# Performance work log

Measured on AMD Instinct MI355X. Metric: run time of the kernel, lower is better.

Reference implementation:

```python
import jax, jax.numpy as jnp
import numpy as np

V = 25; NE = 5; DIM = 192; H = 6; HD = 32; N = 64; T = 64
SCALE = HD ** -0.5
COEFF = 0.4
NTU_EDGES = [(1,2),(2,21),(3,21),(4,3),(5,21),(6,5),(7,6),(8,7),(9,21),(10,9),(11,10),(12,11),(13,1),(14,13),(15,14),(16,15),(17,1),(18,17),(19,18),(20,19),(22,23),(23,8),(24,25),(25,12)]

def _compute_hops():
    # replicate MHSA.__init__ hop-distance computation (A = [I, adj, adj] summed+binarized)
    adj = np.zeros((V, V))
    for i, j in NTU_EDGES:
        adj[i-1, j-1] = 1.0; adj[j-1, i-1] = 1.0
    h1 = ((np.eye(V) + adj) != 0).astype(np.float64)
    h = [None] * V
    h[0] = np.eye(V); h[1] = h1
    hops = np.zeros((V, V))
    for i in range(2, V):
        h[i] = ((h[i-1] @ h1.T) != 0).astype(np.float64)
    for i in range(V-1, 0, -1):
        if np.any(h[i] - h[i-1]):
            h[i] = h[i] - h[i-1]
            hops += i * h[i]
    return hops.astype(np.int32)

def setup_inputs() -> dict:
    key = jax.random.key(0)
    ks = jax.random.split(key, 12)
    hops = jnp.asarray(_compute_hops())
    n_hop = int(hops.max()) + 1
    std = 0.02
    return {
        "x": jax.random.normal(ks[0], (N, DIM, T, V), jnp.float32),
        "joint_label": jnp.arange(V, dtype=jnp.int32) % NE,  # all 5 hyperedge labels present
        "groups": NE,  # unused by forward (kept for signature fidelity)
        "he_weight": jax.random.uniform(ks[1], (NE,), jnp.float32),
        "hops": hops,
        "ln_g": jnp.ones((DIM,), jnp.float32),
        "ln_b": jnp.zeros((DIM,), jnp.float32),
        "hgc_w": std * jax.random.normal(ks[2], (DIM, DIM), jnp.float32),
        "q_w": std * jax.random.normal(ks[3], (DIM, DIM), jnp.float32),
        "kv_w": std * jax.random.normal(ks[4], (2 * DIM, DIM), jnp.float32),
        "proj_w": std * jax.random.normal(ks[5], (DIM, HD), jnp.float32),  # grouped 1x1 conv, groups=6
        "proj_b": jnp.zeros((DIM,), jnp.float32),
        "rpe": std * jax.random.normal(ks[6], (n_hop, DIM), jnp.float32),
        "w1": std * jax.random.normal(ks[7], (H, HD), jnp.float32),
        "outer": jnp.tile(jnp.eye(V, dtype=jnp.float32), (H, 1, 1)) + std * jax.random.normal(ks[8], (H, V, V), jnp.float32),
        "alpha": 0.1 * jnp.ones((1,), jnp.float32),
        "lin1_w": std * jax.random.normal(ks[9], (T // 5, T), jnp.float32),
        "lin1_b": jnp.zeros((T // 5,), jnp.float32),
        "lin2_w": std * jax.random.normal(ks[10], (T, T // 5), jnp.float32),
        "lin2_b": jnp.zeros((T,), jnp.float32),
    }

def _forward(x, joint_label, he_weight, hops, ln_g, ln_b, hgc_w, q_w, kv_w, proj_w, proj_b, rpe, w1, outer, alpha, lin1_w, lin1_b, lin2_w, lin2_b):
    N_, C, T_, V_ = x.shape
    # ---- HGattn branch: hypergraph conv + temporal squeeze-excite gate ----
    label = jax.nn.one_hot(joint_label, NE, dtype=x.dtype)            # (V, 5)
    label1 = label / label.sum(0, keepdims=True)
    label1 = label1 / jnp.sqrt(label.sum(1, keepdims=True))
    label1 = (he_weight[None, :] * label1).T                          # (5, V)
    norm_label = label / label.sum(1, keepdims=True)
    h_adj = norm_label @ label1                                       # (V, V)
    z = jnp.einsum('nctv,vw->nctw', x, h_adj)
    op = jnp.einsum('nctv,oc->notv', z, hgc_w)                        # (N, dim, T, V) 1x1 conv
    op_tr = op.transpose(0, 1, 3, 2)                                  # (N, dim, V, T)
    s = op_tr.mean(axis=(1, 2))                                       # (N, T) global avg pool over (dim, V)
    g = jax.nn.sigmoid(jax.nn.relu(s @ lin1_w.T + lin1_b) @ lin2_w.T + lin2_b)  # (N, T)
    op_final = op_tr + COEFF * (op_tr * g[:, None, None, :])
    e = op_final.transpose(0, 1, 3, 2)                                # (N, dim, T, V)
    # ---- LayerNorm over channel dim ----
    xc = x.transpose(0, 2, 3, 1)                                      # (N, T, V, C)
    mu = xc.mean(-1, keepdims=True)
    var = xc.var(-1, keepdims=True)
    xn = (((xc - mu) / jnp.sqrt(var + 1e-5)) * ln_g + ln_b).transpose(0, 3, 1, 2)
    # ---- MHSA with hop-indexed relative bias, e-branch scores, outer fusion ----
    q = jnp.einsum('nctv,oc->notv', xn, q_w).reshape(N_, H, HD, T_, V_).transpose(0, 3, 1, 4, 2)   # (N,T,H,V,hd)
    kv = jnp.einsum('nctv,oc->notv', xn, kv_w).reshape(N_, 2, H, HD, T_, V_)
    k = kv[:, 0].transpose(0, 3, 1, 4, 2)
    v = kv[:, 1].transpose(0, 3, 1, 4, 2)
    e_k = e.reshape(N_, H, HD, T_, V_).transpose(0, 3, 1, 4, 2)
    k_r = rpe[hops].reshape(V_, V_, H, HD)                            # hop-distance relative position table
    b = jnp.einsum('bthnc,nmhc->bthnm', q, k_r)
    c = jnp.einsum('bthnc,bthmc->bthnm', q, e_k)
    d = jnp.einsum('hc,bthmc->bthm', w1, e_k)[..., None, :]
    a = jnp.einsum('bthnc,bthmc->bthnm', q, k)
    attn = jax.nn.softmax((a + b + c + d) * SCALE, axis=-1)
    o = jnp.einsum('bthnm,bthmc->bthnc', alpha * attn + outer[None, None], v)
    o = o.transpose(0, 1, 2, 4, 3).reshape(N_, T_, DIM, V_).transpose(0, 2, 1, 3)  # (N, dim, T, V)
    # grouped 1x1 conv projection (groups = H)
    og = o.reshape(N_, H, HD, T_, V_)
    wg = proj_w.reshape(H, HD, HD)
    o = jnp.einsum('ngitv,goi->ngotv', og, wg).reshape(N_, DIM, T_, V_) + proj_b[None, :, None, None]
    return x + o  # dim_in == dim -> identity skip

def reference(x, joint_label, groups, he_weight, hops, ln_g, ln_b, hgc_w, q_w, kv_w, proj_w, proj_b, rpe, w1, outer, alpha, lin1_w, lin1_b, lin2_w, lin2_b):
    return _forward(x, joint_label, he_weight, hops, ln_g, ln_b, hgc_w, q_w, kv_w, proj_w, proj_b, rpe, w1, outer, alpha, lin1_w, lin1_b, lin2_w, lin2_b)
```

## Files before the change

### kernel.cpp

```cpp
#include <hip/hip_runtime.h>
#include <hip/hip_bf16.h>

using bf16 = __hip_bfloat16;
typedef __bf16 bf16x8 __attribute__((ext_vector_type(8)));
typedef float f32x4 __attribute__((ext_vector_type(4)));

constexpr int kDim = 192;
constexpr int kH = 6;
constexpr int kHd = 32;
constexpr int kN = 64;
constexpr int kT = 64;
constexpr int kV = 25;
constexpr int kP = kT * kV;
constexpr int kNCstride = kDim * kP;
constexpr float kScale = 0.17677669529663687f;
constexpr float kCoeff = 0.4f;

__global__ void __launch_bounds__(256) setup_kernel(
    const int* __restrict__ jl, const float* __restrict__ hew,
    const float* __restrict__ hgc, const float* __restrict__ qw,
    const float* __restrict__ kvw, const float* __restrict__ rpe,
    const float* __restrict__ proj_w, const float* __restrict__ lng,
    const float* __restrict__ lnb, int n_hop, float* __restrict__ hadj,
    bf16* __restrict__ Wb, float* __restrict__ G, float* __restrict__ Bb,
    bf16* __restrict__ RPEb, bf16* __restrict__ pwb, bf16* __restrict__ VT) {
  const int bid = blockIdx.x;
  const int tid = threadIdx.x;
  if (bid < 576) {
    int i = bid * 256 + tid;
    float v;
    if (i < 36864) {
      v = hgc[i];
    } else {
      int local = i - 36864;
      int c = local % kDim;
      v = (local < 36864) ? qw[local] : kvw[local - 36864];
      v *= lng[c];
    }
    Wb[i] = __float2bfloat16(v);
  } else if (bid == 576) {
    __shared__ int lbl[kV];
    __shared__ int cnt[8];
    if (tid < 8) cnt[tid] = 0;
    __syncthreads();
    if (tid < kV) { lbl[tid] = jl[tid]; atomicAdd(&cnt[lbl[tid]], 1); }
    __syncthreads();
    for (int idx = tid; idx < kV * kV; idx += 256) {
      int v = idx / kV, w = idx - v * kV;
      float val = 0.f;
      if (lbl[v] == lbl[w]) val = hew[lbl[v]] / (float)cnt[lbl[v]];
      hadj[idx] = val;
    }
  } else if (bid == 577) {
    for (int i = tid; i < kH * 16 * kHd; i += 256) {
      int h = i >> 9, hp = (i >> 5) & 15, d = i & 31;
      float v = (hp < n_hop) ? rpe[hp * kDim + h * kHd + d] : 0.f;
      RPEb[i] = __float2bfloat16(v);
    }
    for (int i = tid; i < kDim * kHd; i += 256)
      pwb[i] = __float2bfloat16(proj_w[i]);
  } else if (bid < 722) {
    int o = (bid - 578) * 4 + (tid >> 6);
    int lane = tid & 63;
    const float* Wr =
        (o < kDim) ? (qw + (size_t)o * kDim) : (kvw + (size_t)(o - kDim) * kDim);
    float gs = 0.f, bs = 0.f;
    for (int c = lane; c < kDim; c += 64) {
      float wv = Wr[c];
      gs += wv * lng[c];
      bs += wv * lnb[c];
    }
    for (int off = 32; off > 0; off >>= 1) {
      gs += __shfl_down(gs, off);
      bs += __shfl_down(bs, off);
    }
    if (lane == 0) { G[o] = gs; Bb[o] = bs; }
  } else {
    int row = (bid - 722) * 256 + tid;
    if (row < kN * kT * kDim) {
      uint4 z = {0u, 0u, 0u, 0u};
      *reinterpret_cast<uint4*>(reinterpret_cast<char*>(VT) + (size_t)row * 64 +
                                48) = z;
    }
  }
}

__global__ void __launch_bounds__(256) prep_kernel(
    const float* __restrict__ x, bf16* __restrict__ XR, float* __restrict__ mu,
    float* __restrict__ rstd) {
  __shared__ float ps[kV][25], ps2[kV][25];
  const int tid = threadIdx.x;
  const int t = blockIdx.x, n = blockIdx.y;
  const float* xb = x + (size_t)n * kNCstride + t * kV;
  size_t ob = ((size_t)n * kP + t * kV) * kDim;
  for (int idx = tid; idx < 600; idx += 256) {
    int p = idx % 25, c8 = idx / 25;
    float a = 0.f, b = 0.f;
    union { uint4 u; __bf16 h[8]; } pk;
#pragma unroll
    for (int i = 0; i < 8; ++i) {
      float v = xb[(size_t)(c8 * 8 + i) * kP + p];
      a += v;
      b += v * v;
      pk.h[i] = (__bf16)v;
    }
    *reinterpret_cast<uint4*>(XR + ob + (size_t)p * kDim + c8 * 8) = pk.u;
    ps[p][c8] = a;
    ps2[p][c8] = b;
  }
  __syncthreads();
  if (tid < kV) {
    float a = 0.f, b = 0.f;
#pragma unroll
    for (int c8 = 0; c8 < 24; ++c8) { a += ps[tid][c8]; b += ps2[tid][c8]; }
    float m = a * (1.f / kDim);
    float var = b * (1.f / kDim) - m * m;
    int gid = n * kP + t * kV + tid;
    mu[gid] = m;
    rstd[gid] = rsqrtf(var + 1e-5f);
  }
}

__global__ void __launch_bounds__(64) gemm_all_kernel(
    const bf16* __restrict__ A, const bf16* __restrict__ B,
    bf16* __restrict__ OP, bf16* __restrict__ QK, bf16* __restrict__ VT,
    const float* __restrict__ muA, const float* __restrict__ rsA,
    const float* __restrict__ G, const float* __restrict__ Bb) {
  int id = blockIdx.x;
  int per = gridDim.x >> 3;
  int wg = (id & 7) * per + (id >> 3);
  int n = wg / 300;
  int rem = wg - n * 300;
  const int pt = rem / 12;
  const int ob = rem % 12;
  const int pb = pt * 64;
  const int l = threadIdx.x;
  B += (size_t)n * kNCstride;
  f32x4 acc[4][4] = {};
  const int lm = l & 15;
  const int lk = (l >> 4) * 8;
  for (int kb = 0; kb < kDim; kb += 32) {
    bf16x8 af[4], bfv[4];
#pragma unroll
    for (int mf = 0; mf < 4; ++mf)
      af[mf] = *reinterpret_cast<const bf16x8*>(
          A + (size_t)(ob * 64 + mf * 16 + lm) * kDim + kb + lk);
#pragma unroll
    for (int nf = 0; nf < 4; ++nf)
      bfv[nf] = *reinterpret_cast<const bf16x8*>(
          B + (size_t)(pb + nf * 16 + lm) * kDim + kb + lk);
#pragma unroll
    for (int mf = 0; mf < 4; ++mf)
#pragma unroll
      for (int nf = 0; nf < 4; ++nf)
        acc[mf][nf] = __builtin_amdgcn_mfma_f32_16x16x32_bf16(
            af[mf], bfv[nf], acc[mf][nf], 0, 0, 0);
  }
  const int r0 = (l >> 4) * 4;
  if (ob < 3) {
    OP += (size_t)n * kP * kDim;
#pragma unroll
    for (int mf = 0; mf < 4; ++mf) {
      const int o0 = ob * 64 + mf * 16 + r0;
#pragma unroll
      for (int nf = 0; nf < 4; ++nf) {
        const int p = pb + nf * 16 + lm;
        union { uint2 u; bf16 b[4]; } pk;
#pragma unroll
        for (int r = 0; r < 4; ++r) pk.b[r] = __float2bfloat16(acc[mf][nf][r]);
        *reinterpret_cast<uint2*>(OP + (size_t)p * kDim + o0) = pk.u;
      }
    }
    return;
  }
  float rsv[4], muv[4];
  int tt[4], vv[4];
#pragma unroll
  for (int nf = 0; nf < 4; ++nf) {
    int p = pb + nf * 16 + lm;
    rsv[nf] = rsA[n * kP + p];
    muv[nf] = muA[n * kP + p];
    tt[nf] = p / 25;
    vv[nf] = p - tt[nf] * 25;
  }
#pragma unroll
  for (int mf = 0; mf < 4; ++mf) {
    const int oq = ob * 64 - 192 + mf * 16 + r0;
    float4 g4 = *reinterpret_cast<const float4*>(G + oq);
    float4 b4 = *reinterpret_cast<const float4*>(Bb + oq);
    float ga[4] = {g4.x, g4.y, g4.z, g4.w};
    float ba[4] = {b4.x, b4.y, b4.z, b4.w};
    if (ob < 9) {
#pragma unroll
      for (int nf = 0; nf < 4; ++nf) {
        const int p = pb + nf * 16 + lm;
        union { uint2 u; bf16 b[4]; } pk;
#pragma unroll
        for (int r = 0; r < 4; ++r)
          pk.b[r] = __float2bfloat16(
              rsv[nf] * (acc[mf][nf][r] - muv[nf] * ga[r]) + ba[r]);
        *reinterpret_cast<uint2*>(QK + ((size_t)n * kP + p) * 384 + oq) = pk.u;
      }
    } else {
#pragma unroll
      for (int nf = 0; nf < 4; ++nf) {
        size_t rowb =
            ((size_t)(n * kT + tt[nf]) * kDim + (oq - 384)) * 32 + vv[nf];
#pragma unroll
        for (int r = 0; r < 4; ++r) {
          float vvv = rsv[nf] * (acc[mf][nf][r] - muv[nf] * ga[r]) + ba[r];
          VT[rowb + (size_t)r * 32] = __float2bfloat16(vvv);
        }
      }
    }
  }
}

__global__ void __launch_bounds__(256) haapply_kernel(
    bf16* __restrict__ OP, const float* __restrict__ hadjg,
    float* __restrict__ s_out) {
  __shared__ ushort tile[kV * kDim];
  __shared__ float ha[640];
  __shared__ float red[4];
  const int tid = threadIdx.x;
  const int t = blockIdx.x, n = blockIdx.y;
  size_t base = ((size_t)n * kP + t * kV) * kDim;
  for (int i = tid; i < kV * kV; i += 256) ha[i] = hadjg[i];
  const uint2* src = reinterpret_cast<const uint2*>(OP + base);
  uint2* dst2 = reinterpret_cast<uint2*>(tile);
  for (int i = tid; i < kV * kDim / 4; i += 256) dst2[i] = src[i];
  __syncthreads();
  float ssum = 0.f;
  for (int idx = tid; idx < 600; idx += 256) {
    int c8 = idx % 24, w = idx / 24;
    float acc[8] = {0.f, 0.f, 0.f, 0.f, 0.f, 0.f, 0.f, 0.f};
    for (int v = 0; v < kV; ++v) {
      float coef = ha[v * kV + w];
      union { uint4 u; __bf16 h[8]; } ld;
      ld.u = *reinterpret_cast<const uint4*>(tile + v * kDim + c8 * 8);
#pragma unroll
      for (int j = 0; j < 8; ++j) acc[j] += coef * (float)ld.h[j];
    }
    union { uint4 u; __bf16 h[8]; } pk;
    float s8 = 0.f;
#pragma unroll
    for (int j = 0; j < 8; ++j) { pk.h[j] = (__bf16)acc[j]; s8 += acc[j]; }
    *reinterpret_cast<uint4*>(OP + base + (size_t)w * kDim + c8 * 8) = pk.u;
    ssum += s8;
  }
  for (int off = 32; off > 0; off >>= 1) ssum += __shfl_down(ssum, off);
  if ((tid & 63) == 0) red[tid >> 6] = ssum;
  __syncthreads();
  if (tid == 0)
    s_out[n * kT + t] = (red[0] + red[1] + red[2] + red[3]) *
                        (1.f / (float)(kDim * kV));
}

__global__ void gate_kernel(const float* __restrict__ s,
                            const float* __restrict__ w1l,
                            const float* __restrict__ b1,
                            const float* __restrict__ w2l,
                            const float* __restrict__ b2,
                            float* __restrict__ gatef) {
  __shared__ float sh[kT];
  __shared__ float hid[12];
  int n = blockIdx.x, t = threadIdx.x;
  sh[t] = s[n * kT + t];
  __syncthreads();
  if (t < 12) {
    float a = b1[t];
    for (int j = 0; j < kT; ++j) a += sh[j] * w1l[t * kT + j];
    hid[t] = fmaxf(a, 0.f);
  }
  __syncthreads();
  float a = b2[t];
  for (int j = 0; j < 12; ++j) a += hid[j] * w2l[t * 12 + j];
  float g = 1.f / (1.f + __expf(-a));
  gatef[n * kT + t] = 1.f + kCoeff * g;
}

__global__ void __launch_bounds__(384) attn_kernel(
    const bf16* __restrict__ QK, const bf16* __restrict__ VT,
    const bf16* __restrict__ OP, const float* __restrict__ gatef,
    const int* __restrict__ hops, const bf16* __restrict__ RPEb,
    const float* __restrict__ w1, const float* __restrict__ outer,
    const float* __restrict__ alpha_p, const bf16* __restrict__ pwb,
    const float* __restrict__ proj_b, const float* __restrict__ x,
    float* __restrict__ out) {
  __shared__ ushort wls[kH][2304];
  const int tid = threadIdx.x;
  const int lane = tid & 63;
  const int h = tid >> 6;
  const int t = blockIdx.x, n = blockIdx.y;
  const int nt = n * kT + t;
  const int lm = lane & 15, g = lane >> 4;
  const bool w1ok = (lm + 16) < kV;

  bf16* Pp = (bf16*)&wls[h][0];
  bf16* OLp = (bf16*)&wls[h][1152];

  const float f = gatef[nt];
  const float alpha = alpha_p[0];
  const bf16* Qbase = QK + (size_t)(nt * kV) * 384;
  const bf16* Ebase = OP + (size_t)(nt * kV) * kDim;
  const int colO = h * kHd + g * 8;

  bf16x8 qf[2], kf[2], ef[2];
#pragma unroll
  for (int mf = 0; mf < 2; ++mf) {
    const bf16* row = Qbase + (size_t)(mf * 16 + lm) * 384;
    qf[mf] = *reinterpret_cast<const bf16x8*>(row + colO);
    kf[mf] = *reinterpret_cast<const bf16x8*>(row + kDim + colO);
    ef[mf] = *reinterpret_cast<const bf16x8*>(
        Ebase + (size_t)(mf * 16 + lm) * kDim + colO);
  }
  bf16x8 rf = *reinterpret_cast<const bf16x8*>(RPEb + (h * 16 + lm) * kHd + g * 8);
  bf16x8 vb[2], pwf[2];
#pragma unroll
  for (int nf = 0; nf < 2; ++nf) {
    vb[nf] = *reinterpret_cast<const bf16x8*>(
        VT + ((size_t)(nt * kDim + h * kHd + nf * 16 + lm)) * 32 + g * 8);
    pwf[nf] = *reinterpret_cast<const bf16x8*>(
        pwb + (h * kHd + nf * 16 + lm) * kHd + g * 8);
  }

  float w1v[8];
  {
    float4 wa = *reinterpret_cast<const float4*>(w1 + h * kHd + g * 8);
    float4 wb = *reinterpret_cast<const float4*>(w1 + h * kHd + g * 8 + 4);
    w1v[0] = wa.x; w1v[1] = wa.y; w1v[2] = wa.z; w1v[3] = wa.w;
    w1v[4] = wb.x; w1v[5] = wb.y; w1v[6] = wb.z; w1v[7] = wb.w;
  }
  float dt[2];
#pragma unroll
  for (int nf = 0; nf < 2; ++nf) {
    float a = 0.f;
#pragma unroll
    for (int j = 0; j < 8; ++j) a += w1v[j] * (float)ef[nf][j];
    a += __shfl_xor(a, 16);
    a += __shfl_xor(a, 32);
    dt[nf] = f * a;
  }

  bf16x8 kef[2];
#pragma unroll
  for (int nf = 0; nf < 2; ++nf)
#pragma unroll
    for (int j = 0; j < 8; ++j)
      kef[nf][j] = (__bf16)((float)kf[nf][j] + f * (float)ef[nf][j]);

  f32x4 aK[2][2] = {};
  f32x4 aR[2] = {};
#pragma unroll
  for (int mf = 0; mf < 2; ++mf) {
#pragma unroll
    for (int nf = 0; nf < 2; ++nf)
      aK[mf][nf] =
          __builtin_amdgcn_mfma_f32_16x16x32_bf16(qf[mf], kef[nf], aK[mf][nf], 0, 0, 0);
    aR[mf] = __builtin_amdgcn_mfma_f32_16x16x32_bf16(qf[mf], rf, aR[mf], 0, 0, 0);
  }

#pragma unroll
  for (int mf = 0; mf < 2; ++mf) {
#pragma unroll
    for (int r = 0; r < 4; ++r) {
      int v = mf * 16 + g * 4 + r;
      int vc = v < kV ? v : kV - 1;
      int hp0 = hops[vc * kV + lm];
      int hp1 = w1ok ? hops[vc * kV + lm + 16] : 0;
      float qr0 = __shfl(aR[mf][r], g * 16 + hp0);
      float qr1 = __shfl(aR[mf][r], g * 16 + hp1);
      float s0 = (aK[mf][0][r] + qr0 + dt[0]) * kScale;
      float s1 = (aK[mf][1][r] + qr1 + dt[1]) * kScale;
      if (!w1ok) s1 = -3.0e38f;
      float m = fmaxf(s0, s1);
#pragma unroll
      for (int d = 1; d < 16; d <<= 1) m = fmaxf(m, __shfl_xor(m, d));
      float e0 = __expf(s0 - m);
      float e1 = w1ok ? __expf(s1 - m) : 0.f;
      float sum = e0 + e1;
#pragma unroll
      for (int d = 1; d < 16; d <<= 1) sum += __shfl_xor(sum, d);
      float inv = alpha / sum;
      float o0 = outer[h * (kV * kV) + vc * kV + lm];
      float o1 = w1ok ? outer[h * (kV * kV) + vc * kV + lm + 16] : 0.f;
      Pp[v * 36 + lm] = __float2bfloat16(e0 * inv + o0);
      Pp[v * 36 + lm + 16] = __float2bfloat16(w1ok ? e1 * inv + o1 : 0.f);
    }
  }

  bf16x8 pa[2];
#pragma unroll
  for (int mf = 0; mf < 2; ++mf)
    pa[mf] = *reinterpret_cast<const bf16x8*>(Pp + (mf * 16 + lm) * 36 + g * 8);
  f32x4 aO[2][2] = {};
#pragma unroll
  for (int mf = 0; mf < 2; ++mf)
#pragma unroll
    for (int nf = 0; nf < 2; ++nf)
      aO[mf][nf] =
          __builtin_amdgcn_mfma_f32_16x16x32_bf16(pa[mf], vb[nf], aO[mf][nf], 0, 0, 0);

#pragma unroll
  for (int mf = 0; mf < 2; ++mf)
#pragma unroll
    for (int nf = 0; nf < 2; ++nf)
#pragma unroll
      for (int r = 0; r < 4; ++r)
        OLp[(mf * 16 + g * 4 + r) * 36 + nf * 16 + lm] =
            __float2bfloat16(aO[mf][nf][r]);

  bf16x8 oa[2];
#pragma unroll
  for (int nf = 0; nf < 2; ++nf)
    oa[nf] = *reinterpret_cast<const bf16x8*>(OLp + (nf * 16 + lm) * 36 + g * 8);
  f32x4 aF[2][2] = {};
#pragma unroll
  for (int mf = 0; mf < 2; ++mf)
#pragma unroll
    for (int nf = 0; nf < 2; ++nf)
      aF[mf][nf] =
          __builtin_amdgcn_mfma_f32_16x16x32_bf16(pwf[mf], oa[nf], aF[mf][nf], 0, 0, 0);

#pragma unroll
  for (int mf = 0; mf < 2; ++mf) {
#pragma unroll
    for (int r = 0; r < 4; ++r) {
      int oo = mf * 16 + g * 4 + r;
      int c = h * kHd + oo;
      float pbv = proj_b[c];
      size_t gbase = (size_t)n * kNCstride + (size_t)c * kP + t * kV;
#pragma unroll
      for (int nf = 0; nf < 2; ++nf) {
        int v = nf * 16 + lm;
        if (v < kV) out[gbase + v] = x[gbase + v] + aF[mf][nf][r] + pbv;
      }
    }
  }
}

extern "C" void kernel_launch(void* const* d_in, const int* in_sizes, int n_in,
                              void* d_out, int out_size, void* d_ws,
                              size_t ws_size, hipStream_t stream) {
  const float* x = (const float*)d_in[0];
  const int* joint_label = (const int*)d_in[1];
  const float* he_weight = (const float*)d_in[3];
  const int* hops = (const int*)d_in[4];
  const float* ln_g = (const float*)d_in[5];
  const float* ln_b = (const float*)d_in[6];
  const float* hgc_w = (const float*)d_in[7];
  const float* q_w = (const float*)d_in[8];
  const float* kv_w = (const float*)d_in[9];
  const float* proj_w = (const float*)d_in[10];
  const float* proj_b = (const float*)d_in[11];
  const float* rpe = (const float*)d_in[12];
  const float* w1 = (const float*)d_in[13];
  const float* outer = (const float*)d_in[14];
  const float* alpha = (const float*)d_in[15];
  const float* lin1_w = (const float*)d_in[16];
  const float* lin1_b = (const float*)d_in[17];
  const float* lin2_w = (const float*)d_in[18];
  const float* lin2_b = (const float*)d_in[19];
  const int n_hop = in_sizes[12] / kDim;

  char* w = (char*)d_ws;
  bf16* QK = (bf16*)w;
  w += (size_t)kN * kP * 2 * kDim * 2;
  bf16* XR = (bf16*)w;
  w += (size_t)kN * kP * kDim * 2;
  bf16* OP = (bf16*)w;
  w += (size_t)kN * kP * kDim * 2;
  w += 65536;
  bf16* VT = (bf16*)w;
  w += (size_t)kN * kT * kDim * 32 * 2;
  bf16* Wb = (bf16*)w;
  w += (size_t)768 * kDim * 2;
  bf16* RPEb = (bf16*)w;
  w += (size_t)kH * 16 * kHd * 2;
  bf16* pwb = (bf16*)w;
  w += (size_t)kDim * kHd * 2;
  float* hadj = (float*)w;
  w += 1024 * 4;
  float* s_ws = (float*)w;
  w += kN * kT * 4;
  float* gatef = (float*)w;
  w += kN * kT * 4;
  float* mu = (float*)w;
  w += (size_t)kN * kP * 4;
  float* rstd = (float*)w;
  w += (size_t)kN * kP * 4;
  float* G = (float*)w;
  w += 576 * 4;
  float* Bb = (float*)w;
  w += 576 * 4;

  hipLaunchKernelGGL(setup_kernel, dim3(3794), dim3(256), 0, stream,
                     joint_label, he_weight, hgc_w, q_w, kv_w, rpe, proj_w,
                     ln_g, ln_b, n_hop, hadj, Wb, G, Bb, RPEb, pwb, VT);
  hipLaunchKernelGGL(prep_kernel, dim3(kT, kN), dim3(256), 0, stream, x, XR,
                     mu, rstd);
  hipLaunchKernelGGL(gemm_all_kernel, dim3(25 * 12 * kN), dim3(64), 0, stream,
                     Wb, XR, OP, QK, VT, mu, rstd, G, Bb);
  hipLaunchKernelGGL(haapply_kernel, dim3(kT, kN), dim3(256), 0, stream, OP,
                     hadj, s_ws);
  hipLaunchKernelGGL(gate_kernel, dim3(kN), dim3(kT), 0, stream, s_ws, lin1_w,
                     lin1_b, lin2_w, lin2_b, gatef);
  hipLaunchKernelGGL(attn_kernel, dim3(kT, kN), dim3(384), 0, stream, QK, VT,
                     OP, gatef, hops, RPEb, w1, outer, alpha, pwb, proj_b, x,
                     (float*)d_out);
}
```

Measured before the change: 354.0 us.

## Group four GEMM waves per block and stage hop gather through LDS

```diff
diff --git a/kernel.cpp b/kernel.cpp
--- a/kernel.cpp
+++ b/kernel.cpp
@@ -121,7 +121,7 @@
   }
 }
 
-__global__ void __launch_bounds__(64) gemm_all_kernel(
+__global__ void __launch_bounds__(256) gemm_all_kernel(
     const bf16* __restrict__ A, const bf16* __restrict__ B,
     bf16* __restrict__ OP, bf16* __restrict__ QK, bf16* __restrict__ VT,
     const float* __restrict__ muA, const float* __restrict__ rsA,
@@ -129,12 +129,13 @@
   int id = blockIdx.x;
   int per = gridDim.x >> 3;
   int wg = (id & 7) * per + (id >> 3);
-  int n = wg / 300;
-  int rem = wg - n * 300;
-  const int pt = rem / 12;
-  const int ob = rem % 12;
+  int n = wg / 75;
+  int rem = wg - n * 75;
+  const int pt = rem / 3;
+  const int obq = rem % 3;
+  const int ob = obq * 4 + (threadIdx.x >> 6);
   const int pb = pt * 64;
-  const int l = threadIdx.x;
+  const int l = threadIdx.x & 63;
   B += (size_t)n * kNCstride;
   f32x4 acc[4][4] = {};
   const int lm = l & 15;
@@ -288,6 +289,7 @@
     const float* __restrict__ proj_b, const float* __restrict__ x,
     float* __restrict__ out) {
   __shared__ ushort wls[kH][2304];
+  __shared__ unsigned char hopsB[kV][32];
   const int tid = threadIdx.x;
   const int lane = tid & 63;
   const int h = tid >> 6;
@@ -296,8 +298,15 @@
   const int lm = lane & 15, g = lane >> 4;
   const bool w1ok = (lm + 16) < kV;
 
+  for (int i = tid; i < kV * 32; i += 384) {
+    int v = i >> 5, w = i & 31;
+    hopsB[v][w] = (w < kV) ? (unsigned char)hops[v * kV + w] : 0;
+  }
+  __syncthreads();
+
   bf16* Pp = (bf16*)&wls[h][0];
   bf16* OLp = (bf16*)&wls[h][1152];
+  float* QRp = (float*)&wls[h][1152];
 
   const float f = gatef[nt];
   const float alpha = alpha_p[0];
@@ -315,14 +324,6 @@
         Ebase + (size_t)(mf * 16 + lm) * kDim + colO);
   }
   bf16x8 rf = *reinterpret_cast<const bf16x8*>(RPEb + (h * 16 + lm) * kHd + g * 8);
-  bf16x8 vb[2], pwf[2];
-#pragma unroll
-  for (int nf = 0; nf < 2; ++nf) {
-    vb[nf] = *reinterpret_cast<const bf16x8*>(
-        VT + ((size_t)(nt * kDim + h * kHd + nf * 16 + lm)) * 32 + g * 8);
-    pwf[nf] = *reinterpret_cast<const bf16x8*>(
-        pwb + (h * kHd + nf * 16 + lm) * kHd + g * 8);
-  }
 
   float w1v[8];
   {
@@ -361,17 +362,21 @@
   }
 
 #pragma unroll
+  for (int mf = 0; mf < 2; ++mf)
+#pragma unroll
+    for (int r = 0; r < 4; ++r)
+      QRp[(mf * 16 + g * 4 + r) * 17 + lm] = aR[mf][r];
+
+#pragma unroll
   for (int mf = 0; mf < 2; ++mf) {
 #pragma unroll
     for (int r = 0; r < 4; ++r) {
       int v = mf * 16 + g * 4 + r;
       int vc = v < kV ? v : kV - 1;
-      int hp0 = hops[vc * kV + lm];
-      int hp1 = w1ok ? hops[vc * kV + lm + 16] : 0;
-      float qr0 = __shfl(aR[mf][r], g * 16 + hp0);
-      float qr1 = __shfl(aR[mf][r], g * 16 + hp1);
-      float s0 = (aK[mf][0][r] + qr0 + dt[0]) * kScale;
-      float s1 = (aK[mf][1][r] + qr1 + dt[1]) * kScale;
+      int hp0 = hopsB[vc][lm];
+      int hp1 = hopsB[vc][lm + 16];
+      float s0 = (aK[mf][0][r] + QRp[v * 17 + hp0] + dt[0]) * kScale;
+      float s1 = (aK[mf][1][r] + QRp[v * 17 + hp1] + dt[1]) * kScale;
       if (!w1ok) s1 = -3.0e38f;
       float m = fmaxf(s0, s1);
 #pragma unroll
@@ -389,10 +394,14 @@
     }
   }
 
-  bf16x8 pa[2];
+  bf16x8 pa[2], vb[2];
 #pragma unroll
   for (int mf = 0; mf < 2; ++mf)
     pa[mf] = *reinterpret_cast<const bf16x8*>(Pp + (mf * 16 + lm) * 36 + g * 8);
+#pragma unroll
+  for (int nf = 0; nf < 2; ++nf)
+    vb[nf] = *reinterpret_cast<const bf16x8*>(
+        VT + ((size_t)(nt * kDim + h * kHd + nf * 16 + lm)) * 32 + g * 8);
   f32x4 aO[2][2] = {};
 #pragma unroll
   for (int mf = 0; mf < 2; ++mf)
@@ -410,10 +419,14 @@
         OLp[(mf * 16 + g * 4 + r) * 36 + nf * 16 + lm] =
             __float2bfloat16(aO[mf][nf][r]);
 
-  bf16x8 oa[2];
+  bf16x8 oa[2], pwf[2];
 #pragma unroll
   for (int nf = 0; nf < 2; ++nf)
     oa[nf] = *reinterpret_cast<const bf16x8*>(OLp + (nf * 16 + lm) * 36 + g * 8);
+#pragma unroll
+  for (int mf = 0; mf < 2; ++mf)
+    pwf[mf] = *reinterpret_cast<const bf16x8*>(pwb +
+        (h * kHd + mf * 16 + lm) * kHd + g * 8);
   f32x4 aF[2][2] = {};
 #pragma unroll
   for (int mf = 0; mf < 2; ++mf)
@@ -499,7 +512,7 @@
                      ln_g, ln_b, n_hop, hadj, Wb, G, Bb, RPEb, pwb, VT);
   hipLaunchKernelGGL(prep_kernel, dim3(kT, kN), dim3(256), 0, stream, x, XR,
                      mu, rstd);
-  hipLaunchKernelGGL(gemm_all_kernel, dim3(25 * 12 * kN), dim3(64), 0, stream,
+  hipLaunchKernelGGL(gemm_all_kernel, dim3(75 * kN), dim3(256), 0, stream,
                      Wb, XR, OP, QK, VT, mu, rstd, G, Bb);
   hipLaunchKernelGGL(haapply_kernel, dim3(kT, kN), dim3(256), 0, stream, OP,
                      hadj, s_ws);
```

Result: no change. 347.9 us (-1.7%).
